# Kernel tuning notes

Measured on AMD Instinct MI355X. Metric: run time of the kernel, lower is better.

The kernel has to match this reference:

```python
import jax, jax.numpy as jnp
import numpy as np

N_NODES = 50000
N_EDGES = 800000
IN_DIM = 128
HID = 128
TIME = 6.0
STEPS = 12


def setup_inputs() -> dict:
    key = jax.random.key(0)
    ks = jax.random.split(key, 8)
    gat_out = jax.random.normal(ks[0], (N_NODES, IN_DIM), dtype=jnp.float32)
    edge_index = jax.random.randint(ks[1], (2, N_EDGES), 0, N_NODES, dtype=jnp.int64)
    # scale weights like PyTorch Linear default (uniform-ish magnitude)
    W_in = jax.random.normal(ks[2], (IN_DIM, HID), dtype=jnp.float32) * (1.0 / np.sqrt(IN_DIM))
    b_in = jnp.zeros((HID,), dtype=jnp.float32)
    W1 = jax.random.normal(ks[3], (HID, 2 * HID), dtype=jnp.float32) * (1.0 / np.sqrt(HID))
    b1 = jnp.zeros((2 * HID,), dtype=jnp.float32)
    W2 = jax.random.normal(ks[4], (2 * HID, HID), dtype=jnp.float32) * (1.0 / np.sqrt(2 * HID))
    b2 = jnp.zeros((HID,), dtype=jnp.float32)
    clearance = jnp.full((1,), 0.1, dtype=jnp.float32)
    return {"gat_out": gat_out, "edge_index": edge_index, "W_in": W_in, "b_in": b_in,
            "W1": W1, "b1": b1, "W2": W2, "b2": b2, "clearance": clearance}


def reference(gat_out, edge_index, W_in, b_in, W1, b1, W2, b2, clearance):
    N = gat_out.shape[0]
    dt = TIME / STEPS
    src, dst = edge_index[0], edge_index[1]
    h = jnp.tanh(gat_out @ W_in + b_in)  # [N, HID]
    # degree is identical each Euler step in the original; hoist it once
    deg = jax.ops.segment_sum(jnp.ones((src.shape[0],), dtype=h.dtype), dst, num_segments=N)
    deg = jnp.clip(deg, 1.0, None)[:, None]  # [N, 1]
    decay = jax.nn.relu(clearance)  # [1]

    def step(h, _):
        agg = jax.ops.segment_sum(h[src], dst, num_segments=N) / deg  # [N, HID]
        diff = jnp.tanh(jax.nn.gelu(agg @ W1 + b1, approximate=False) @ W2 + b2)
        h = h + (diff - decay * h) * dt
        return h, None

    h, _ = jax.lax.scan(step, h, None, length=STEPS)
    return h
```

## Files before the change

kernel.cpp:

```cpp
#include <hip/hip_runtime.h>
#include <math.h>

#define N_NODES 50000
#define N_EDGES 800000
#define HID 128
#define H2 256
#define STEPS 12
#define DT 0.5f

#define SCAN_B 256
#define NB ((N_NODES + SCAN_B - 1) / SCAN_B)
#define NODE_BLOCKS ((N_NODES + 31) / 32)
#define N_PAD (NODE_BLOCKS * 32)
#define CSR_CAP (N_EDGES + 4 * N_NODES)

typedef __attribute__((ext_vector_type(8))) short bf16x8;
typedef __attribute__((ext_vector_type(4))) float f32x4;

__device__ inline unsigned short f2bf(float x) {
    unsigned int u = __float_as_uint(x);
    unsigned int r = (u + 0x7FFFu + ((u >> 16) & 1u)) >> 16;
    return (unsigned short)r;
}
__device__ inline float bf2f(unsigned short b) {
    return __uint_as_float(((unsigned int)b) << 16);
}
__device__ inline float u2f(unsigned int u) { return __uint_as_float(u); }

__device__ inline float fast_tanh(float x) {
    float xc = fminf(fmaxf(x, -9.0f), 9.0f);
    float t = __builtin_amdgcn_exp2f(xc * 2.8853900817779268f);
    return 1.0f - 2.0f * __builtin_amdgcn_rcpf(t + 1.0f);
}

__device__ inline float fast_gelu(float x) {
    float u  = x * 0.70710678118654752f;
    float au = fabsf(u);
    float t  = __builtin_amdgcn_rcpf(fmaf(0.3275911f, au, 1.0f));
    float poly = t * (0.254829592f + t * (-0.284496736f + t * (1.421413741f +
                 t * (-1.453152027f + t * 1.061405429f))));
    float ex = __builtin_amdgcn_exp2f(-au * au * 1.4426950408889634f);
    float erfv = copysignf(1.0f - poly * ex, u);
    return 0.5f * x * (1.0f + erfv);
}


__global__ void k_zero_counts(int* __restrict__ counts) {
    int i = blockIdx.x * 256 + threadIdx.x;
    if (i < N_NODES) counts[i] = 0;
}

__global__ void k_fill_csr(int* __restrict__ csr) {
    int i = blockIdx.x * 256 + threadIdx.x;
    if (i < CSR_CAP) csr[i] = N_NODES;
}

__global__ void k_zero_padrows(unsigned short* __restrict__ a, unsigned short* __restrict__ b) {
    int i = blockIdx.x * 256 + threadIdx.x;
    if (i < (N_PAD - N_NODES) * HID) {
        a[(size_t)N_NODES * HID + i] = 0;
        b[(size_t)N_NODES * HID + i] = 0;
    }
}

__global__ void k_hist(const int* __restrict__ dst, int* __restrict__ counts) {
    int e = blockIdx.x * 256 + threadIdx.x;
    if (e < N_EDGES) atomicAdd(&counts[dst[e]], 1);
}

__global__ void k_blocksum(const int* __restrict__ counts, int* __restrict__ bsum) {
    __shared__ int s[SCAN_B];
    int idx = blockIdx.x * SCAN_B + threadIdx.x;
    int v = (idx < N_NODES) ? ((counts[idx] + 3) & ~3) : 0;
    s[threadIdx.x] = v;
    __syncthreads();
    for (int off = SCAN_B / 2; off > 0; off >>= 1) {
        if (threadIdx.x < off) s[threadIdx.x] += s[threadIdx.x + off];
        __syncthreads();
    }
    if (threadIdx.x == 0) bsum[blockIdx.x] = s[0];
}

__global__ void k_scan_bsums(int* __restrict__ bsum, int* __restrict__ offsets) {
    __shared__ int s[SCAN_B];
    int tid = threadIdx.x;
    int v = (tid < NB) ? bsum[tid] : 0;
    s[tid] = v;
    __syncthreads();
    for (int off = 1; off < SCAN_B; off <<= 1) {
        int t = 0;
        if (tid >= off) t = s[tid - off];
        __syncthreads();
        s[tid] += t;
        __syncthreads();
    }
    if (tid < NB) bsum[tid] = s[tid] - v;
    if (tid == SCAN_B - 1) offsets[N_NODES] = s[SCAN_B - 1];
}

__global__ void k_offsets(const int* __restrict__ counts, const int* __restrict__ bsum,
                          int* __restrict__ offsets, int* __restrict__ cursor) {
    __shared__ int s[SCAN_B];
    int idx = blockIdx.x * SCAN_B + threadIdx.x;
    int v = (idx < N_NODES) ? ((counts[idx] + 3) & ~3) : 0;
    s[threadIdx.x] = v;
    __syncthreads();
    for (int off = 1; off < SCAN_B; off <<= 1) {
        int t = 0;
        if ((int)threadIdx.x >= off) t = s[threadIdx.x - off];
        __syncthreads();
        s[threadIdx.x] += t;
        __syncthreads();
    }
    if (idx < N_NODES) {
        int excl = s[threadIdx.x] - v;
        int o = bsum[blockIdx.x] + excl;
        offsets[idx] = o;
        cursor[idx]  = o;
    }
}

__global__ void k_scatter(const int* __restrict__ src, const int* __restrict__ dst,
                          int* __restrict__ cursor, int* __restrict__ csr_src) {
    int e = blockIdx.x * 256 + threadIdx.x;
    if (e < N_EDGES) {
        int d = dst[e];
        int p = atomicAdd(&cursor[d], 1);
        csr_src[p] = src[e];
    }
}


__global__ void k_pack(const float* __restrict__ W, int K, int N,
                       unsigned short* __restrict__ hi, unsigned short* __restrict__ lo) {
    int KT = K >> 5, NT = N >> 4;
    int t = blockIdx.x * 256 + threadIdx.x;
    if (t >= KT * NT * 64) return;
    int l = t & 63, tile = t >> 6;
    int kt = tile % KT, nt = tile / KT;
    int n  = nt * 16 + (l & 15);
    int k0 = kt * 32 + (l >> 4) * 8;
    int base = ((nt * KT + kt) * 64 + l) * 8;
    for (int j = 0; j < 8; j++) {
        float w = W[(size_t)(k0 + j) * N + n];
        unsigned short h = f2bf(w);
        hi[base + j] = h;
        lo[base + j] = f2bf(w - bf2f(h));
    }
}


__global__ __launch_bounds__(256, 3) void k_h0_mfma(
    const float* __restrict__ gat,
    const unsigned short* __restrict__ wh, const unsigned short* __restrict__ wl,
    const float* __restrict__ b_in, float* __restrict__ h,
    unsigned short* __restrict__ hbf) {
    __shared__ unsigned short Ahi[32][136];
    __shared__ unsigned short Alo[32][136];
    int tid = threadIdx.x;
    int node0 = blockIdx.x * 32;

    for (int idx = tid; idx < 32 * 64; idx += 256) {
        int m = idx >> 6, c = (idx & 63) * 2;
        float2 v;
        if (node0 + m < N_NODES) v = *(const float2*)&gat[(size_t)(node0 + m) * 128 + c];
        else { v.x = 0.f; v.y = 0.f; }
        unsigned short h0 = f2bf(v.x), h1 = f2bf(v.y);
        unsigned short l0 = f2bf(v.x - bf2f(h0)), l1 = f2bf(v.y - bf2f(h1));
        *(unsigned int*)&Ahi[m][c] = (unsigned int)h0 | ((unsigned int)h1 << 16);
        *(unsigned int*)&Alo[m][c] = (unsigned int)l0 | ((unsigned int)l1 << 16);
    }
    __syncthreads();

    int l = tid & 63, wv = tid >> 6;
    int c15 = l & 15, q = l >> 4;
    f32x4 acc[2][2] = {};
#pragma unroll
    for (int kt = 0; kt < 4; kt++) {
        bf16x8 ah[2], al[2];
#pragma unroll
        for (int mt = 0; mt < 2; mt++) {
            ah[mt] = *(const bf16x8*)&Ahi[mt * 16 + c15][kt * 32 + q * 8];
            al[mt] = *(const bf16x8*)&Alo[mt * 16 + c15][kt * 32 + q * 8];
        }
#pragma unroll
        for (int nn = 0; nn < 2; nn++) {
            int nt = wv * 2 + nn;
            bf16x8 bh = *(const bf16x8*)&wh[(size_t)((nt * 4 + kt) * 64 + l) * 8];
            bf16x8 bl = *(const bf16x8*)&wl[(size_t)((nt * 4 + kt) * 64 + l) * 8];
#pragma unroll
            for (int mt = 0; mt < 2; mt++) {
                acc[mt][nn] = __builtin_amdgcn_mfma_f32_16x16x32_bf16(ah[mt], bh, acc[mt][nn], 0, 0, 0);
                acc[mt][nn] = __builtin_amdgcn_mfma_f32_16x16x32_bf16(ah[mt], bl, acc[mt][nn], 0, 0, 0);
                acc[mt][nn] = __builtin_amdgcn_mfma_f32_16x16x32_bf16(al[mt], bh, acc[mt][nn], 0, 0, 0);
            }
        }
    }
#pragma unroll
    for (int nn = 0; nn < 2; nn++) {
        int col = (wv * 2 + nn) * 16 + c15;
        float bb = b_in[col];
#pragma unroll
        for (int mt = 0; mt < 2; mt++)
#pragma unroll
            for (int r = 0; r < 4; r++) {
                int node = node0 + mt * 16 + q * 4 + r;
                if (node < N_NODES) {
                    float v = fast_tanh(acc[mt][nn][r] + bb);
                    h[(size_t)node * 128 + col]   = v;
                    hbf[(size_t)node * 128 + col] = f2bf(v);
                }
            }
    }
}


#define ACC8(V) \
    a0 += u2f((V).x << 16); a1 += u2f((V).x & 0xFFFF0000u); \
    a2 += u2f((V).y << 16); a3 += u2f((V).y & 0xFFFF0000u); \
    a4 += u2f((V).z << 16); a5 += u2f((V).z & 0xFFFF0000u); \
    a6 += u2f((V).w << 16); a7 += u2f((V).w & 0xFFFF0000u);

__global__ __launch_bounds__(512, 4) void k_step(
    const unsigned short* __restrict__ hbf_in,
    float* __restrict__ h, unsigned short* __restrict__ hbf_out,
    const int* __restrict__ offsets, const int* __restrict__ csr,
    const int* __restrict__ cnt,
    const unsigned short* __restrict__ w1h, const unsigned short* __restrict__ w1l,
    const float* __restrict__ b1,
    const unsigned short* __restrict__ w2h, const unsigned short* __restrict__ w2l,
    const float* __restrict__ b2, const float* __restrict__ clr) {
    __shared__ unsigned short Ahi[32][136];
    __shared__ unsigned short Alo[32][136];
    __shared__ unsigned short Y[32][264];
    int tid = threadIdx.x, l = tid & 63, wv = tid >> 6;
    int c15 = l & 15, q = l >> 4;
    int node0 = blockIdx.x * 32;
    int g  = l >> 4;
    int cl = l & 15;

    {
        int m = wv * 4 + g;
        int node = node0 + m;
        float a0 = 0.f, a1 = 0.f, a2 = 0.f, a3 = 0.f;
        float a4 = 0.f, a5 = 0.f, a6 = 0.f, a7 = 0.f;
        int deg = 0;
        if (node < N_NODES) {
            int beg = offsets[node], end = offsets[node + 1];
            deg = cnt[node];
            const unsigned short* hb = hbf_in + cl * 8;
            if (beg < end) {
                int4 ii = *(const int4*)&csr[beg];
                for (int e = beg; e < end; e += 4) {
                    int enx = (e + 4 < end) ? (e + 4) : e;
                    int4 iin = *(const int4*)&csr[enx];
                    uint4 w0 = *(const uint4*)&hb[((unsigned)ii.x) << 7];
                    uint4 w1 = *(const uint4*)&hb[((unsigned)ii.y) << 7];
                    uint4 w2 = *(const uint4*)&hb[((unsigned)ii.z) << 7];
                    uint4 w3 = *(const uint4*)&hb[((unsigned)ii.w) << 7];
                    ii = iin;
                    ACC8(w0); ACC8(w1); ACC8(w2); ACC8(w3);
                }
            }
        }
        float inv = (deg > 1) ? 1.0f / (float)deg : 1.0f;
        float x0 = a0 * inv, x1 = a1 * inv, x2 = a2 * inv, x3 = a3 * inv;
        float x4 = a4 * inv, x5 = a5 * inv, x6 = a6 * inv, x7 = a7 * inv;
        unsigned short h0 = f2bf(x0), h1 = f2bf(x1), h2 = f2bf(x2), h3 = f2bf(x3);
        unsigned short h4 = f2bf(x4), h5 = f2bf(x5), h6 = f2bf(x6), h7 = f2bf(x7);
        uint4 ohi;
        ohi.x = (unsigned int)h0 | ((unsigned int)h1 << 16);
        ohi.y = (unsigned int)h2 | ((unsigned int)h3 << 16);
        ohi.z = (unsigned int)h4 | ((unsigned int)h5 << 16);
        ohi.w = (unsigned int)h6 | ((unsigned int)h7 << 16);
        *(uint4*)&Ahi[m][cl * 8] = ohi;
        unsigned short l0 = f2bf(x0 - bf2f(h0)), l1 = f2bf(x1 - bf2f(h1));
        unsigned short l2 = f2bf(x2 - bf2f(h2)), l3 = f2bf(x3 - bf2f(h3));
        unsigned short l4 = f2bf(x4 - bf2f(h4)), l5 = f2bf(x5 - bf2f(h5));
        unsigned short l6 = f2bf(x6 - bf2f(h6)), l7 = f2bf(x7 - bf2f(h7));
        uint4 olo;
        olo.x = (unsigned int)l0 | ((unsigned int)l1 << 16);
        olo.y = (unsigned int)l2 | ((unsigned int)l3 << 16);
        olo.z = (unsigned int)l4 | ((unsigned int)l5 << 16);
        olo.w = (unsigned int)l6 | ((unsigned int)l7 << 16);
        *(uint4*)&Alo[m][cl * 8] = olo;
    }
    __syncthreads();

    {
        f32x4 acc1[2][2] = {};
#pragma unroll
        for (int kt = 0; kt < 4; kt++) {
            bf16x8 ah[2], al[2];
#pragma unroll
            for (int mt = 0; mt < 2; mt++) {
                ah[mt] = *(const bf16x8*)&Ahi[mt * 16 + c15][kt * 32 + q * 8];
                al[mt] = *(const bf16x8*)&Alo[mt * 16 + c15][kt * 32 + q * 8];
            }
#pragma unroll
            for (int nn = 0; nn < 2; nn++) {
                int nt = wv * 2 + nn;
                bf16x8 bh = *(const bf16x8*)&w1h[(size_t)((nt * 4 + kt) * 64 + l) * 8];
                bf16x8 bl = *(const bf16x8*)&w1l[(size_t)((nt * 4 + kt) * 64 + l) * 8];
#pragma unroll
                for (int mt = 0; mt < 2; mt++) {
                    acc1[mt][nn] = __builtin_amdgcn_mfma_f32_16x16x32_bf16(ah[mt], bh, acc1[mt][nn], 0, 0, 0);
                    acc1[mt][nn] = __builtin_amdgcn_mfma_f32_16x16x32_bf16(ah[mt], bl, acc1[mt][nn], 0, 0, 0);
                    acc1[mt][nn] = __builtin_amdgcn_mfma_f32_16x16x32_bf16(al[mt], bh, acc1[mt][nn], 0, 0, 0);
                }
            }
        }
#pragma unroll
        for (int nn = 0; nn < 2; nn++) {
            int col = (wv * 2 + nn) * 16 + c15;
            float bb = b1[col];
#pragma unroll
            for (int mt = 0; mt < 2; mt++)
#pragma unroll
                for (int r = 0; r < 4; r++) {
                    int row = mt * 16 + q * 4 + r;
                    float x = acc1[mt][nn][r] + bb;
                    Y[row][col] = f2bf(fast_gelu(x));
                }
        }
    }
    __syncthreads();

    f32x4 acc2[2] = {};
#pragma unroll
    for (int kt = 0; kt < 8; kt++) {
        bf16x8 ya[2];
#pragma unroll
        for (int mt = 0; mt < 2; mt++)
            ya[mt] = *(const bf16x8*)&Y[mt * 16 + c15][kt * 32 + q * 8];
        bf16x8 bh = *(const bf16x8*)&w2h[(size_t)((wv * 8 + kt) * 64 + l) * 8];
        bf16x8 bl = *(const bf16x8*)&w2l[(size_t)((wv * 8 + kt) * 64 + l) * 8];
#pragma unroll
        for (int mt = 0; mt < 2; mt++) {
            acc2[mt] = __builtin_amdgcn_mfma_f32_16x16x32_bf16(ya[mt], bh, acc2[mt], 0, 0, 0);
            acc2[mt] = __builtin_amdgcn_mfma_f32_16x16x32_bf16(ya[mt], bl, acc2[mt], 0, 0, 0);
        }
    }
    float decay = fmaxf(clr[0], 0.0f);
    {
        int col = wv * 16 + c15;
        float bb = b2[col];
#pragma unroll
        for (int mt = 0; mt < 2; mt++)
#pragma unroll
            for (int r = 0; r < 4; r++) {
                int node = node0 + mt * 16 + q * 4 + r;
                if (node < N_NODES) {
                    float hv = h[(size_t)node * 128 + col];
                    float diff = fast_tanh(acc2[mt][r] + bb);
                    float nh = hv + (diff - decay * hv) * DT;
                    h[(size_t)node * 128 + col]       = nh;
                    hbf_out[(size_t)node * 128 + col] = f2bf(nh);
                }
            }
    }
}


extern "C" void kernel_launch(void* const* d_in, const int* in_sizes, int n_in,
                              void* d_out, int out_size, void* d_ws, size_t ws_size,
                              hipStream_t stream) {
    const float* gat   = (const float*)d_in[0];
    const int*   edges = (const int*)d_in[1];
    const float* W_in  = (const float*)d_in[2];
    const float* b_in  = (const float*)d_in[3];
    const float* W1    = (const float*)d_in[4];
    const float* b1    = (const float*)d_in[5];
    const float* W2    = (const float*)d_in[6];
    const float* b2    = (const float*)d_in[7];
    const float* clr   = (const float*)d_in[8];
    float* h = (float*)d_out;

    const int* src = edges;
    const int* dst = edges + N_EDGES;

    char* ws = (char*)d_ws;
    size_t off = 0;
    auto alloc = [&](size_t bytes) -> void* {
        off = (off + 255) & ~(size_t)255;
        void* p = ws + off;
        off += bytes;
        return p;
    };
    int*   counts  = (int*)alloc(sizeof(int) * N_NODES);
    int*   offsets = (int*)alloc(sizeof(int) * (N_NODES + 1));
    int*   cursor  = (int*)alloc(sizeof(int) * N_NODES);
    int*   bsum    = (int*)alloc(sizeof(int) * NB);
    int*   csr_src = (int*)alloc(sizeof(int) * CSR_CAP);
    unsigned short* hbfA = (unsigned short*)alloc(sizeof(short) * (size_t)N_PAD * HID);
    unsigned short* hbfB = (unsigned short*)alloc(sizeof(short) * (size_t)N_PAD * HID);
    unsigned short* w1h  = (unsigned short*)alloc(sizeof(short) * HID * H2);
    unsigned short* w1l  = (unsigned short*)alloc(sizeof(short) * HID * H2);
    unsigned short* w2h  = (unsigned short*)alloc(sizeof(short) * H2 * HID);
    unsigned short* w2l  = (unsigned short*)alloc(sizeof(short) * H2 * HID);
    unsigned short* winh = (unsigned short*)alloc(sizeof(short) * HID * HID);
    unsigned short* winl = (unsigned short*)alloc(sizeof(short) * HID * HID);

    k_pack<<<16, 256, 0, stream>>>(W1, 128, 256, w1h, w1l);
    k_pack<<<16, 256, 0, stream>>>(W2, 256, 128, w2h, w2l);
    k_pack<<<8, 256, 0, stream>>>(W_in, 128, 128, winh, winl);

    k_zero_counts<<<NB, 256, 0, stream>>>(counts);
    k_fill_csr<<<(CSR_CAP + 255) / 256, 256, 0, stream>>>(csr_src);
    k_zero_padrows<<<8, 256, 0, stream>>>(hbfA, hbfB);
    k_hist<<<(N_EDGES + 255) / 256, 256, 0, stream>>>(dst, counts);
    k_blocksum<<<NB, 256, 0, stream>>>(counts, bsum);
    k_scan_bsums<<<1, SCAN_B, 0, stream>>>(bsum, offsets);
    k_offsets<<<NB, 256, 0, stream>>>(counts, bsum, offsets, cursor);
    k_scatter<<<(N_EDGES + 255) / 256, 256, 0, stream>>>(src, dst, cursor, csr_src);

    k_h0_mfma<<<NODE_BLOCKS, 256, 0, stream>>>(gat, winh, winl, b_in, h, hbfA);

    for (int s = 0; s < STEPS; s++) {
        const unsigned short* in = (s & 1) ? hbfB : hbfA;
        unsigned short*      out = (s & 1) ? hbfA : hbfB;
        k_step<<<NODE_BLOCKS, 512, 0, stream>>>(in, h, out, offsets, csr_src, counts,
                                                w1h, w1l, b1, w2h, w2l, b2, clr);
    }
}
```

Measured before the change: 861.8 us.

## Merge CSR setup kernels, replace scan with atomic offsets, deepen gather prefetch

Three init kernels become one, and the three-kernel prefix scan is replaced by a single kernel that hands out per-node segment offsets with atomicAdd on a global cursor. Segments are therefore in arbitrary order rather than sorted. The step kernel now derives each segment length from the degree instead of offsets[node+1], and it software-pipelines the neighbor-row gather by loading the next chunk's rows before accumulating the current ones. The aims are fewer kernel launches and more memory-level parallelism in the gather, at the cost of lost locality in the CSR layout and more registers.

```diff
diff --git a/kernel.cpp b/kernel.cpp
--- a/kernel.cpp
+++ b/kernel.cpp
@@ -8,8 +8,7 @@
 #define STEPS 12
 #define DT 0.5f
 
-#define SCAN_B 256
-#define NB ((N_NODES + SCAN_B - 1) / SCAN_B)
+#define NB ((N_NODES + 255) / 256)
 #define NODE_BLOCKS ((N_NODES + 31) / 32)
 #define N_PAD (NODE_BLOCKS * 32)
 #define CSR_CAP (N_EDGES + 4 * N_NODES)
@@ -45,18 +44,13 @@
 }
 
 
-__global__ void k_zero_counts(int* __restrict__ counts) {
+__global__ void k_init(int* __restrict__ counts, int* __restrict__ gcur,
+                       int* __restrict__ csr,
+                       unsigned short* __restrict__ a, unsigned short* __restrict__ b) {
     int i = blockIdx.x * 256 + threadIdx.x;
+    if (i == 0) *gcur = 0;
     if (i < N_NODES) counts[i] = 0;
-}
-
-__global__ void k_fill_csr(int* __restrict__ csr) {
-    int i = blockIdx.x * 256 + threadIdx.x;
     if (i < CSR_CAP) csr[i] = N_NODES;
-}
-
-__global__ void k_zero_padrows(unsigned short* __restrict__ a, unsigned short* __restrict__ b) {
-    int i = blockIdx.x * 256 + threadIdx.x;
     if (i < (N_PAD - N_NODES) * HID) {
         a[(size_t)N_NODES * HID + i] = 0;
         b[(size_t)N_NODES * HID + i] = 0;
@@ -68,55 +62,14 @@
     if (e < N_EDGES) atomicAdd(&counts[dst[e]], 1);
 }
 
-__global__ void k_blocksum(const int* __restrict__ counts, int* __restrict__ bsum) {
-    __shared__ int s[SCAN_B];
-    int idx = blockIdx.x * SCAN_B + threadIdx.x;
-    int v = (idx < N_NODES) ? ((counts[idx] + 3) & ~3) : 0;
-    s[threadIdx.x] = v;
-    __syncthreads();
-    for (int off = SCAN_B / 2; off > 0; off >>= 1) {
-        if (threadIdx.x < off) s[threadIdx.x] += s[threadIdx.x + off];
-        __syncthreads();
-    }
-    if (threadIdx.x == 0) bsum[blockIdx.x] = s[0];
-}
-
-__global__ void k_scan_bsums(int* __restrict__ bsum, int* __restrict__ offsets) {
-    __shared__ int s[SCAN_B];
-    int tid = threadIdx.x;
-    int v = (tid < NB) ? bsum[tid] : 0;
-    s[tid] = v;
-    __syncthreads();
-    for (int off = 1; off < SCAN_B; off <<= 1) {
-        int t = 0;
-        if (tid >= off) t = s[tid - off];
-        __syncthreads();
-        s[tid] += t;
-        __syncthreads();
-    }
-    if (tid < NB) bsum[tid] = s[tid] - v;
-    if (tid == SCAN_B - 1) offsets[N_NODES] = s[SCAN_B - 1];
-}
-
-__global__ void k_offsets(const int* __restrict__ counts, const int* __restrict__ bsum,
-                          int* __restrict__ offsets, int* __restrict__ cursor) {
-    __shared__ int s[SCAN_B];
-    int idx = blockIdx.x * SCAN_B + threadIdx.x;
-    int v = (idx < N_NODES) ? ((counts[idx] + 3) & ~3) : 0;
-    s[threadIdx.x] = v;
-    __syncthreads();
-    for (int off = 1; off < SCAN_B; off <<= 1) {
-        int t = 0;
-        if ((int)threadIdx.x >= off) t = s[threadIdx.x - off];
-        __syncthreads();
-        s[threadIdx.x] += t;
-        __syncthreads();
-    }
-    if (idx < N_NODES) {
-        int excl = s[threadIdx.x] - v;
-        int o = bsum[blockIdx.x] + excl;
-        offsets[idx] = o;
-        cursor[idx]  = o;
+__global__ void k_offsets_atomic(const int* __restrict__ counts, int* __restrict__ gcur,
+                                 int* __restrict__ offsets, int* __restrict__ cursor) {
+    int i = blockIdx.x * 256 + threadIdx.x;
+    if (i < N_NODES) {
+        int p = (counts[i] + 3) & ~3;
+        int o = atomicAdd(gcur, p);
+        offsets[i] = o;
+        cursor[i]  = o;
     }
 }
 
@@ -246,21 +199,29 @@
         float a4 = 0.f, a5 = 0.f, a6 = 0.f, a7 = 0.f;
         int deg = 0;
         if (node < N_NODES) {
-            int beg = offsets[node], end = offsets[node + 1];
             deg = cnt[node];
+            int beg = offsets[node];
+            int nch = ((deg + 3) & ~3) >> 2;
             const unsigned short* hb = hbf_in + cl * 8;
-            if (beg < end) {
-                int4 ii = *(const int4*)&csr[beg];
-                for (int e = beg; e < end; e += 4) {
-                    int enx = (e + 4 < end) ? (e + 4) : e;
-                    int4 iin = *(const int4*)&csr[enx];
-                    uint4 w0 = *(const uint4*)&hb[((unsigned)ii.x) << 7];
-                    uint4 w1 = *(const uint4*)&hb[((unsigned)ii.y) << 7];
-                    uint4 w2 = *(const uint4*)&hb[((unsigned)ii.z) << 7];
-                    uint4 w3 = *(const uint4*)&hb[((unsigned)ii.w) << 7];
-                    ii = iin;
-                    ACC8(w0); ACC8(w1); ACC8(w2); ACC8(w3);
-                }
+            const int* cp = &csr[beg];
+            if (nch > 0) {
+                int4 ii = *(const int4*)cp;
+                int4 ij = (nch > 1) ? *(const int4*)(cp + 4) : ii;
+                uint4 r0 = *(const uint4*)&hb[((unsigned)ii.x) << 7];
+                uint4 r1 = *(const uint4*)&hb[((unsigned)ii.y) << 7];
+                uint4 r2 = *(const uint4*)&hb[((unsigned)ii.z) << 7];
+                uint4 r3 = *(const uint4*)&hb[((unsigned)ii.w) << 7];
+                for (int c = 0; c + 1 < nch; c++) {
+                    uint4 n0 = *(const uint4*)&hb[((unsigned)ij.x) << 7];
+                    uint4 n1 = *(const uint4*)&hb[((unsigned)ij.y) << 7];
+                    uint4 n2 = *(const uint4*)&hb[((unsigned)ij.z) << 7];
+                    uint4 n3 = *(const uint4*)&hb[((unsigned)ij.w) << 7];
+                    int4 ik = (c + 2 < nch) ? *(const int4*)(cp + (c + 2) * 4) : ij;
+                    ACC8(r0); ACC8(r1); ACC8(r2); ACC8(r3);
+                    r0 = n0; r1 = n1; r2 = n2; r3 = n3;
+                    ij = ik;
+                }
+                ACC8(r0); ACC8(r1); ACC8(r2); ACC8(r3);
             }
         }
         float inv = (deg > 1) ? 1.0f / (float)deg : 1.0f;
@@ -388,9 +349,9 @@
         return p;
     };
     int*   counts  = (int*)alloc(sizeof(int) * N_NODES);
-    int*   offsets = (int*)alloc(sizeof(int) * (N_NODES + 1));
+    int*   offsets = (int*)alloc(sizeof(int) * N_NODES);
     int*   cursor  = (int*)alloc(sizeof(int) * N_NODES);
-    int*   bsum    = (int*)alloc(sizeof(int) * NB);
+    int*   gcur    = (int*)alloc(sizeof(int));
     int*   csr_src = (int*)alloc(sizeof(int) * CSR_CAP);
     unsigned short* hbfA = (unsigned short*)alloc(sizeof(short) * (size_t)N_PAD * HID);
     unsigned short* hbfB = (unsigned short*)alloc(sizeof(short) * (size_t)N_PAD * HID);
@@ -405,13 +366,9 @@
     k_pack<<<16, 256, 0, stream>>>(W2, 256, 128, w2h, w2l);
     k_pack<<<8, 256, 0, stream>>>(W_in, 128, 128, winh, winl);
 
-    k_zero_counts<<<NB, 256, 0, stream>>>(counts);
-    k_fill_csr<<<(CSR_CAP + 255) / 256, 256, 0, stream>>>(csr_src);
-    k_zero_padrows<<<8, 256, 0, stream>>>(hbfA, hbfB);
+    k_init<<<(CSR_CAP + 255) / 256, 256, 0, stream>>>(counts, gcur, csr_src, hbfA, hbfB);
     k_hist<<<(N_EDGES + 255) / 256, 256, 0, stream>>>(dst, counts);
-    k_blocksum<<<NB, 256, 0, stream>>>(counts, bsum);
-    k_scan_bsums<<<1, SCAN_B, 0, stream>>>(bsum, offsets);
-    k_offsets<<<NB, 256, 0, stream>>>(counts, bsum, offsets, cursor);
+    k_offsets_atomic<<<NB, 256, 0, stream>>>(counts, gcur, offsets, cursor);
     k_scatter<<<(N_EDGES + 255) / 256, 256, 0, stream>>>(src, dst, cursor, csr_src);
 
     k_h0_mfma<<<NODE_BLOCKS, 256, 0, stream>>>(gat, winh, winl, b_in, h, hbfA);
```

After: 947.8 us. 1.1x slower.
